# Performance work log

Measured on AMD Instinct MI355X. Metric: run time of the kernel, lower is better.

The kernel has to match this reference:

```python
import jax, jax.numpy as jnp
import numpy as np
import math

B, S, HID, H = 4, 2048, 1024, 16
D = HID // H


def setup_inputs() -> dict:
    key = jax.random.key(0)
    ks = jax.random.split(key, 13)
    xavier = lambda k: jax.random.normal(k, (HID, HID), jnp.float32) * math.sqrt(2.0 / (HID + HID))
    return {
        "q": jax.random.normal(ks[0], (B, S, HID), jnp.float32),
        "k": jax.random.normal(ks[1], (B, S, HID), jnp.float32),
        "v": jax.random.normal(ks[2], (B, S, HID), jnp.float32),
        "padding_mask": jax.random.randint(ks[3], (B, S), 0, 2, jnp.int32),
        "Wq": xavier(ks[4]), "bq": jnp.zeros((HID,), jnp.float32),
        "Wk": xavier(ks[5]), "bk": jnp.zeros((HID,), jnp.float32),
        "Wv": xavier(ks[6]), "bv": jnp.zeros((HID,), jnp.float32),
        "Wo": xavier(ks[7]), "bo": jnp.zeros((HID,), jnp.float32),
        "is_causal": 1,
    }


def reference(q, k, v, padding_mask, Wq, bq, Wk, bk, Wv, bv, Wo, bo, is_causal):
    b, s, _ = q.shape
    # torch Linear: y = x @ W.T + b; reshape to [B, H, S, D]
    proj = lambda x, W, bias: (x @ W.T + bias).reshape(b, s, H, D).transpose(0, 2, 1, 3)
    qh, kh, vh = proj(q, Wq, bq), proj(k, Wk, bk), proj(v, Wv, bv)
    corr = jnp.einsum("bhqd,bhkd->bhqk", qh, kh) / math.sqrt(D)  # [B,H,S,S]
    # padding_mask.view(B,1,S,1): masks QUERY rows where mask == 0 (faithful to source)
    corr = jnp.where(padding_mask[:, None, :, None] == 0, jnp.float32(-1e9), corr)
    if is_causal:
        # triu -inf above diagonal; where(...) equals corr + (-inf) at masked slots
        tri = jnp.triu(jnp.ones((s, s), bool), k=1)
        corr = jnp.where(tri[None, None], -jnp.inf, corr)
    prob = jax.nn.softmax(corr, axis=-1)  # dropout p=0 (eval)
    hidden = jnp.einsum("bhqk,bhkd->bhqd", prob, vh)  # [B,H,S,D]
    hidden = hidden.transpose(0, 2, 1, 3).reshape(b, s, H * D)
    return hidden @ Wo.T + bo
```

## Files before the change

### kernel.cpp

```cpp
#include <hip/hip_runtime.h>
#include <hip/hip_bf16.h>
#include <stdint.h>

typedef __attribute__((ext_vector_type(8))) short bf16x8;
typedef __attribute__((ext_vector_type(4))) float f32x4;
typedef __attribute__((ext_vector_type(16))) float f32x16;
typedef __attribute__((ext_vector_type(8))) unsigned short ushort8;
typedef __attribute__((ext_vector_type(4))) unsigned short ushort4v;
typedef __attribute__((ext_vector_type(4))) unsigned int u32x4;
typedef __attribute__((ext_vector_type(2))) unsigned int u32x2;

#define DEVINL __device__ __forceinline__

static constexpr int BB  = 4;
static constexpr int SS  = 2048;
static constexpr int HID = 1024;
static constexpr int NH  = 16;
static constexpr int DH  = 64;

DEVINL unsigned short f2bf(float f) {
  unsigned u = __builtin_bit_cast(unsigned, f);
  u += 0x7fffu + ((u >> 16) & 1u);
  return (unsigned short)(u >> 16);
}

DEVINL unsigned cvt_pk_bf16(float lo, float hi) {
  unsigned r;
  asm("v_cvt_pk_bf16_f32 %0, %1, %2" : "=v"(r) : "v"(lo), "v"(hi));
  return r;
}

DEVINL void gload_lds16(const void* g, void* lds) {
  __builtin_amdgcn_global_load_lds(
      (__attribute__((address_space(1))) unsigned int*)(g),
      (__attribute__((address_space(3))) unsigned int*)(lds), 16, 0, 0);
}

__global__ void cvt4_weights(const float* __restrict__ a,
                             const float* __restrict__ b,
                             const float* __restrict__ c,
                             const float* __restrict__ d,
                             unsigned short* __restrict__ dst) {
  int which = blockIdx.x >> 9;
  const float* src = which == 0 ? a : which == 1 ? b : which == 2 ? c : d;
  int i = ((blockIdx.x & 511) * 256 + threadIdx.x) * 8;
  float4 v0 = *(const float4*)(src + i);
  float4 v1 = *(const float4*)(src + i + 4);
  ushort8 h;
  h[0] = f2bf(v0.x); h[1] = f2bf(v0.y); h[2] = f2bf(v0.z); h[3] = f2bf(v0.w);
  h[4] = f2bf(v1.x); h[5] = f2bf(v1.y); h[6] = f2bf(v1.z); h[7] = f2bf(v1.w);
  *(ushort8*)(dst + which * 1048576 + i) = h;
}

__launch_bounds__(256)
__global__ void gemm_qkv(const float* __restrict__ qp,
                         const float* __restrict__ kp,
                         const float* __restrict__ vp,
                         const unsigned short* __restrict__ W,
                         const float* __restrict__ bq,
                         const float* __restrict__ bk,
                         const float* __restrict__ bv,
                         unsigned short* __restrict__ dstQK,
                         unsigned short* __restrict__ Vt, float sclq) {
  __shared__ __align__(16) unsigned char As[16384];
  __shared__ __align__(16) unsigned char Bs[2][16384];
  const int cpx = gridDim.x >> 3;
  const int bid = (blockIdx.x & 7) * cpx + (blockIdx.x >> 3);
  const int which = bid / 512;
  const int tile = bid - which * 512;
  const int bm = tile >> 3, bn = tile & 7;
  const int m0 = bm << 7, n0 = bn << 7;
  const int K = 1024, N = 1024;
  const float* Af = which == 0 ? qp : which == 1 ? kp : vp;
  const unsigned short* Bw = W + which * 1048576;
  const float* bias = which == 0 ? bq : which == 1 ? bk : bv;
  const float osc = which == 0 ? sclq : 1.0f;

  const int t = threadIdx.x, lane = t & 63, wv = t >> 6;
  const int wr = wv >> 1, wc = wv & 1;
  const int l15 = lane & 15, l4 = lane >> 4;

  f32x4 acc[4][4] = {};
  float4 ar[8];

  auto LOAD_A = [&](int k0) {
#pragma unroll
    for (int j = 0; j < 8; ++j) {
      int qid = t + j * 256;
      int row = qid >> 4;
      int q16 = qid & 15;
      ar[j] = *(const float4*)(Af + (size_t)(m0 + row) * K + k0 + q16 * 4);
    }
  };
  auto WRITE_A = [&]() {
#pragma unroll
    for (int j = 0; j < 8; ++j) {
      int qid = t + j * 256;
      int row = qid >> 4;
      int q16 = qid & 15;
      u32x2 w;
      w.x = cvt_pk_bf16(ar[j].x, ar[j].y);
      w.y = cvt_pk_bf16(ar[j].z, ar[j].w);
      int byte = (row * 128 + q16 * 8) ^ ((row & 7) << 4);
      *(u32x2*)(As + byte) = w;
    }
  };
  auto STAGE_B = [&](int k0, int s) {
#pragma unroll
    for (int j = 0; j < 4; ++j) {
      int p = (wv * 4 + j) * 1024 + lane * 16;
      int row = p >> 7;
      int cb = (p & 127) ^ ((row & 7) << 4);
      gload_lds16(Bw + (size_t)(n0 + row) * K + k0 + (cb >> 1),
                  Bs[s] + (wv * 4 + j) * 1024);
    }
  };

  LOAD_A(0);
  STAGE_B(0, 0);
  const int nk = K >> 6;
  for (int i = 0; i < nk; ++i) {
    const int s = i & 1;
    WRITE_A();
    if (i + 1 < nk) {
      LOAD_A((i + 1) << 6);
      STAGE_B((i + 1) << 6, s ^ 1);
      asm volatile("s_waitcnt vmcnt(12) lgkmcnt(0)" ::: "memory");
    } else {
      asm volatile("s_waitcnt vmcnt(0) lgkmcnt(0)" ::: "memory");
    }
    __builtin_amdgcn_s_barrier();

    bf16x8 af[2][4], bfr[2][4];
#pragma unroll
    for (int kh = 0; kh < 2; ++kh) {
#pragma unroll
      for (int m = 0; m < 4; ++m) {
        int r = wr * 64 + m * 16 + l15;
        int byte = (r * 128 + kh * 64 + l4 * 16) ^ ((r & 7) << 4);
        af[kh][m] = *(const bf16x8*)(As + byte);
      }
#pragma unroll
      for (int n = 0; n < 4; ++n) {
        int r = wc * 64 + n * 16 + l15;
        int byte = (r * 128 + kh * 64 + l4 * 16) ^ ((r & 7) << 4);
        bfr[kh][n] = *(const bf16x8*)(Bs[s] + byte);
      }
    }
#pragma unroll
    for (int kh = 0; kh < 2; ++kh)
#pragma unroll
      for (int m = 0; m < 4; ++m)
#pragma unroll
        for (int n = 0; n < 4; ++n)
          acc[m][n] = __builtin_amdgcn_mfma_f32_16x16x32_bf16(
              af[kh][m], bfr[kh][n], acc[m][n], 0, 0, 0);

    asm volatile("s_waitcnt lgkmcnt(0)" ::: "memory");
    __builtin_amdgcn_s_barrier();
  }

  if (which < 2) {
    unsigned short* Cp = dstQK + (size_t)which * 8388608;
#pragma unroll
    for (int n = 0; n < 4; ++n) {
      int col = n0 + wc * 64 + n * 16 + l15;
      float bc = bias[col];
#pragma unroll
      for (int m = 0; m < 4; ++m) {
        int rowb = m0 + wr * 64 + m * 16 + l4 * 4;
#pragma unroll
        for (int r = 0; r < 4; ++r) {
          float val = (acc[m][n][r] + bc) * osc;
          Cp[(size_t)(rowb + r) * N + col] = f2bf(val);
        }
      }
    }
  } else {
#pragma unroll
    for (int n = 0; n < 4; ++n) {
      int dcol = n0 + wc * 64 + n * 16 + l15;
      float bc = bias[dcol];
#pragma unroll
      for (int m = 0; m < 4; ++m) {
        int srow = m0 + wr * 64 + m * 16 + l4 * 4;
        int bb = srow >> 11, s = srow & 2047;
        ushort4v o;
#pragma unroll
        for (int r = 0; r < 4; ++r) o[r] = f2bf(acc[m][n][r] + bc);
        *(ushort4v*)(Vt + ((size_t)(bb * 1024 + dcol)) * 2048 + s) = o;
      }
    }
  }
}

__launch_bounds__(256)
__global__ void gemm_out(const unsigned short* __restrict__ Ab,
                         const unsigned short* __restrict__ Bw,
                         const float* __restrict__ bias,
                         float* __restrict__ Cp, int M, int N, int K) {
  __shared__ __align__(16) unsigned char As[2][16384];
  __shared__ __align__(16) unsigned char Bs[2][16384];
  const int cpx = gridDim.x >> 3;
  const int bid = (blockIdx.x & 7) * cpx + (blockIdx.x >> 3);
  const int nb = N >> 7;
  const int bm = bid / nb, bn = bid % nb;
  const int m0 = bm << 7, n0 = bn << 7;
  const int t = threadIdx.x, lane = t & 63, wv = t >> 6;
  const int wr = wv >> 1, wc = wv & 1;
  const int l15 = lane & 15, l4 = lane >> 4;

  f32x4 acc[4][4] = {};

  auto STAGE = [&](int k0, int s) {
#pragma unroll
    for (int j = 0; j < 4; ++j) {
      int p = (wv * 4 + j) * 1024 + lane * 16;
      int row = p >> 7;
      int cb = (p & 127) ^ ((row & 7) << 4);
      gload_lds16(Bw + (size_t)(n0 + row) * K + k0 + (cb >> 1),
                  Bs[s] + (wv * 4 + j) * 1024);
      gload_lds16(Ab + (size_t)(m0 + row) * K + k0 + (cb >> 1),
                  As[s] + (wv * 4 + j) * 1024);
    }
  };

  STAGE(0, 0);
  const int nk = K >> 6;
  for (int i = 0; i < nk; ++i) {
    const int s = i & 1;
    if (i + 1 < nk) {
      STAGE((i + 1) << 6, s ^ 1);
      asm volatile("s_waitcnt vmcnt(8)" ::: "memory");
    } else {
      asm volatile("s_waitcnt vmcnt(0)" ::: "memory");
    }
    __builtin_amdgcn_s_barrier();

    bf16x8 af[2][4], bfr[2][4];
#pragma unroll
    for (int kh = 0; kh < 2; ++kh) {
#pragma unroll
      for (int m = 0; m < 4; ++m) {
        int r = wr * 64 + m * 16 + l15;
        int byte = (r * 128 + kh * 64 + l4 * 16) ^ ((r & 7) << 4);
        af[kh][m] = *(const bf16x8*)(As[s] + byte);
      }
#pragma unroll
      for (int n = 0; n < 4; ++n) {
        int r = wc * 64 + n * 16 + l15;
        int byte = (r * 128 + kh * 64 + l4 * 16) ^ ((r & 7) << 4);
        bfr[kh][n] = *(const bf16x8*)(Bs[s] + byte);
      }
    }
#pragma unroll
    for (int kh = 0; kh < 2; ++kh)
#pragma unroll
      for (int m = 0; m < 4; ++m)
#pragma unroll
        for (int n = 0; n < 4; ++n)
          acc[m][n] = __builtin_amdgcn_mfma_f32_16x16x32_bf16(
              af[kh][m], bfr[kh][n], acc[m][n], 0, 0, 0);

    asm volatile("s_waitcnt lgkmcnt(0)" ::: "memory");
    __builtin_amdgcn_s_barrier();
  }

#pragma unroll
  for (int n = 0; n < 4; ++n) {
    int col = n0 + wc * 64 + n * 16 + l15;
    float bc = bias[col];
#pragma unroll
    for (int m = 0; m < 4; ++m) {
      int rowb = m0 + wr * 64 + m * 16 + l4 * 4;
#pragma unroll
      for (int r = 0; r < 4; ++r)
        Cp[(size_t)(rowb + r) * N + col] = acc[m][n][r] + bc;
    }
  }
}

__launch_bounds__(256)
__global__ void attn_kernel(const unsigned short* __restrict__ Qh,
                            const unsigned short* __restrict__ Kh,
                            const unsigned short* __restrict__ Vt,
                            const int* __restrict__ pad,
                            const int* __restrict__ pcausal,
                            unsigned short* __restrict__ Out) {
  __shared__ __align__(16) unsigned char Ks[2][16384];
  __shared__ __align__(16) unsigned char Vs[2][16384];
  const int bid = (blockIdx.x & 7) * 64 + (blockIdx.x >> 3);
  const int pr = bid & 7, h = (bid >> 3) & 15, b = bid >> 7;
  const int t = threadIdx.x, lane = t & 63, wv = t >> 6;
  const int l31 = lane & 31, hi = lane >> 5;
  const int causal = *pcausal;

  for (int half = 0; half < 2; ++half) {
    const int qt = half ? (15 - pr) : pr;
    const int q0 = qt << 7;
    const int qrow = q0 + wv * 32 + l31;
    const bool padded = (pad[b * SS + qrow] == 0);

    const unsigned short* Qb = Qh + ((size_t)(b * SS) + qrow) * HID + h * DH;
    bf16x8 qf[4];
#pragma unroll
    for (int dd = 0; dd < 4; ++dd) {
      qf[dd] = *(const bf16x8*)(Qb + dd * 16 + hi * 8);
      if (padded) qf[dd] = (bf16x8)0;
    }

    f32x16 oacc[2] = {};
    float m = -__builtin_inff(), l = 0.f;
    const int nkt = causal ? (qt + 1) : (SS >> 7);

    auto STAGE = [&](int kt, int s) {
#pragma unroll
      for (int j = 0; j < 4; ++j) {
        int p = (wv * 4 + j) * 1024 + lane * 16;
        int kr = p >> 7;
        int kcb = (p & 127) ^ ((kr & 7) << 4);
        gload_lds16(Kh + ((size_t)(b * SS) + (kt << 7) + kr) * HID + h * DH +
                        (kcb >> 1),
                    Ks[s] + (wv * 4 + j) * 1024);
        int vr = p >> 8;
        int vcb = (p & 255) ^ ((vr & 15) << 4);
        gload_lds16(Vt + ((size_t)((b * NH + h) * DH + vr)) * SS + (kt << 7) +
                        (vcb >> 1),
                    Vs[s] + (wv * 4 + j) * 1024);
      }
    };

    if (half) __syncthreads();
    STAGE(0, 0);
    for (int kt = 0; kt < nkt; ++kt) {
      asm volatile("s_waitcnt vmcnt(0)" ::: "memory");
      __syncthreads();
      if (kt + 1 < nkt) STAGE(kt + 1, (kt + 1) & 1);
      const unsigned char* Kb = Ks[kt & 1];
      const unsigned char* Vb = Vs[kt & 1];

#pragma unroll
      for (int sub = 0; sub < 2; ++sub) {
        const int k0 = (kt << 7) + (sub << 6);
        const bool active = (!causal) || (k0 <= q0 + wv * 32 + 31);
        if (!active) continue;
        f32x16 sacc[2] = {};
#pragma unroll
        for (int kb = 0; kb < 2; ++kb) {
#pragma unroll
          for (int dd = 0; dd < 4; ++dd) {
            int krow = sub * 64 + kb * 32 + l31;
            int byte = (krow * 128 + dd * 32 + hi * 16) ^ ((krow & 7) << 4);
            bf16x8 kf = *(const bf16x8*)(Kb + byte);
            sacc[kb] = __builtin_amdgcn_mfma_f32_32x32x16_bf16(kf, qf[dd],
                                                               sacc[kb], 0, 0, 0);
          }
        }
        if (causal && (k0 + 63 > q0 + wv * 32)) {
#pragma unroll
          for (int kb = 0; kb < 2; ++kb)
#pragma unroll
            for (int r = 0; r < 16; ++r) {
              int kidx = k0 + kb * 32 + (r & 3) + 8 * (r >> 2) + 4 * hi;
              if (kidx > qrow) sacc[kb][r] = -__builtin_inff();
            }
        }
        float ta = fmaxf(sacc[0][0], sacc[0][1]);
        float tb = fmaxf(sacc[0][2], sacc[0][3]);
#pragma unroll
        for (int r = 4; r < 16; r += 4) {
          ta = fmaxf(ta, fmaxf(sacc[0][r], sacc[0][r + 1]));
          tb = fmaxf(tb, fmaxf(sacc[0][r + 2], sacc[0][r + 3]));
        }
#pragma unroll
        for (int r = 0; r < 16; r += 4) {
          ta = fmaxf(ta, fmaxf(sacc[1][r], sacc[1][r + 1]));
          tb = fmaxf(tb, fmaxf(sacc[1][r + 2], sacc[1][r + 3]));
        }
        float tmax = fmaxf(ta, tb);
        tmax = fmaxf(tmax, __shfl_xor(tmax, 32));
        if (__any(tmax > m + 8.0f)) {
          float mnew = fmaxf(m, tmax);
          float corr = __builtin_amdgcn_exp2f(m - mnew);
          m = mnew;
          l *= corr;
#pragma unroll
          for (int db = 0; db < 2; ++db)
#pragma unroll
            for (int r = 0; r < 16; ++r) oacc[db][r] *= corr;
        }
        float ls = 0.f;
#pragma unroll
        for (int kb = 0; kb < 2; ++kb)
#pragma unroll
          for (int r = 0; r < 16; ++r) {
            float p = __builtin_amdgcn_exp2f(sacc[kb][r] - m);
            sacc[kb][r] = p;
            ls += p;
          }
        l += ls;

        bf16x8 pf[4];
#pragma unroll
        for (int kb = 0; kb < 2; ++kb) {
          unsigned w0 = cvt_pk_bf16(sacc[kb][0], sacc[kb][1]);
          unsigned w1 = cvt_pk_bf16(sacc[kb][2], sacc[kb][3]);
          unsigned w2 = cvt_pk_bf16(sacc[kb][4], sacc[kb][5]);
          unsigned w3 = cvt_pk_bf16(sacc[kb][6], sacc[kb][7]);
          unsigned w4 = cvt_pk_bf16(sacc[kb][8], sacc[kb][9]);
          unsigned w5 = cvt_pk_bf16(sacc[kb][10], sacc[kb][11]);
          unsigned w6 = cvt_pk_bf16(sacc[kb][12], sacc[kb][13]);
          unsigned w7 = cvt_pk_bf16(sacc[kb][14], sacc[kb][15]);
          unsigned t0 = __shfl_xor(hi ? w0 : w2, 32);
          unsigned t1 = __shfl_xor(hi ? w1 : w3, 32);
          unsigned t2 = __shfl_xor(hi ? w4 : w6, 32);
          unsigned t3 = __shfl_xor(hi ? w5 : w7, 32);
          u32x4 lo, hf;
          lo[0] = hi ? t0 : w0;
          lo[1] = hi ? t1 : w1;
          lo[2] = hi ? w2 : t0;
          lo[3] = hi ? w3 : t1;
          hf[0] = hi ? t2 : w4;
          hf[1] = hi ? t3 : w5;
          hf[2] = hi ? w6 : t2;
          hf[3] = hi ? w7 : t3;
          pf[2 * kb] = __builtin_bit_cast(bf16x8, lo);
          pf[2 * kb + 1] = __builtin_bit_cast(bf16x8, hf);
        }
#pragma unroll
        for (int db = 0; db < 2; ++db) {
#pragma unroll
          for (int kk = 0; kk < 4; ++kk) {
            int drow = db * 32 + l31;
            int byte = (drow * 256 + sub * 128 + kk * 32 + hi * 16) ^
                       ((drow & 15) << 4);
            bf16x8 vf = *(const bf16x8*)(Vb + byte);
            oacc[db] = __builtin_amdgcn_mfma_f32_32x32x16_bf16(vf, pf[kk],
                                                               oacc[db], 0, 0, 0);
          }
        }
      }
    }

    float ltot = l + __shfl_xor(l, 32);
    float inv = 1.0f / ltot;
    size_t rowoff = ((size_t)(b * SS) + qrow) * HID + h * DH;
#pragma unroll
    for (int db = 0; db < 2; ++db) {
#pragma unroll
      for (int g = 0; g < 4; ++g) {
        ushort4v o;
#pragma unroll
        for (int j = 0; j < 4; ++j) o[j] = f2bf(oacc[db][4 * g + j] * inv);
        *(ushort4v*)(Out + rowoff + db * 32 + 8 * g + 4 * hi) = o;
      }
    }
  }
}

extern "C" void kernel_launch(void* const* d_in, const int* in_sizes, int n_in,
                              void* d_out, int out_size, void* d_ws,
                              size_t ws_size, hipStream_t stream) {
  const float* q = (const float*)d_in[0];
  const float* k = (const float*)d_in[1];
  const float* v = (const float*)d_in[2];
  const int* pad = (const int*)d_in[3];
  const float* Wq = (const float*)d_in[4];
  const float* bq = (const float*)d_in[5];
  const float* Wk = (const float*)d_in[6];
  const float* bk = (const float*)d_in[7];
  const float* Wv = (const float*)d_in[8];
  const float* bv = (const float*)d_in[9];
  const float* Wo = (const float*)d_in[10];
  const float* bo = (const float*)d_in[11];
  const int* iscausal = (const int*)d_in[12];
  float* out = (float*)d_out;

  const float SCL = 0.18033688011112042f;
  const int NQKV = BB * SS * HID;

  unsigned short* Wcat = (unsigned short*)d_ws;
  unsigned short* Wob = Wcat + 3145728;
  unsigned short* Qh = Wob + 1048576;
  unsigned short* Kh = Qh + (size_t)NQKV;
  unsigned short* Vtp = Kh + (size_t)NQKV;
  unsigned short* Htmp = Vtp + (size_t)NQKV;

  cvt4_weights<<<2048, 256, 0, stream>>>(Wq, Wk, Wv, Wo, Wcat);

  gemm_qkv<<<1536, 256, 0, stream>>>(q, k, v, Wcat, bq, bk, bv, Qh, Vtp, SCL);

  attn_kernel<<<512, 256, 0, stream>>>(Qh, Kh, Vtp, pad, iscausal, Htmp);

  gemm_out<<<512, 256, 0, stream>>>(Htmp, Wob, bo, out, 8192, 1024, 1024);
}
```

Before: 179.0 us.

## Pre-convert QKV activations to bf16 and use double-buffered bf16 projection GEMMs

Adds a kernel that converts the fp32 q/k/v activations to bf16 up front, plus a new GEMM that streams both operands into double-buffered LDS with async global-to-LDS loads. It replaces the fused fp32-input QKV projection with three launches of that GEMM, one per projection, when the workspace is large enough. The aim is to halve the operand bytes the GEMM loads and to pipeline both operands, instead of converting fp32 A tiles inside the GEMM. The cost is an extra full read and write pass over the activations, more kernel launches and a larger workspace requirement. The old path is kept as a fallback.

After: 192.1 us. 1.07x slower.

```diff
diff --git a/kernel.cpp b/kernel.cpp
--- a/kernel.cpp
+++ b/kernel.cpp
@@ -50,6 +50,129 @@
   h[0] = f2bf(v0.x); h[1] = f2bf(v0.y); h[2] = f2bf(v0.z); h[3] = f2bf(v0.w);
   h[4] = f2bf(v1.x); h[5] = f2bf(v1.y); h[6] = f2bf(v1.z); h[7] = f2bf(v1.w);
   *(ushort8*)(dst + which * 1048576 + i) = h;
+}
+
+__global__ void cvt_qkv3(const float* __restrict__ q,
+                         const float* __restrict__ k,
+                         const float* __restrict__ v,
+                         unsigned short* __restrict__ dst) {
+  int which = blockIdx.x >> 12;
+  const float* src = which == 0 ? q : which == 1 ? k : v;
+  int i = ((blockIdx.x & 4095) * 256 + threadIdx.x) * 8;
+  float4 v0 = *(const float4*)(src + i);
+  float4 v1 = *(const float4*)(src + i + 4);
+  ushort8 h;
+  h[0] = f2bf(v0.x); h[1] = f2bf(v0.y); h[2] = f2bf(v0.z); h[3] = f2bf(v0.w);
+  h[4] = f2bf(v1.x); h[5] = f2bf(v1.y); h[6] = f2bf(v1.z); h[7] = f2bf(v1.w);
+  *(ushort8*)(dst + (size_t)which * 8388608 + i) = h;
+}
+
+__launch_bounds__(256)
+__global__ void gemm_b(const unsigned short* __restrict__ Ab,
+                       const unsigned short* __restrict__ Bw,
+                       const float* __restrict__ bias,
+                       unsigned short* __restrict__ dstN,
+                       unsigned short* __restrict__ dstT,
+                       int mode, float osc) {
+  __shared__ __align__(16) unsigned char As[2][16384];
+  __shared__ __align__(16) unsigned char Bs[2][16384];
+  const int K = 1024, N = 1024;
+  const int cpx = gridDim.x >> 3;
+  const int bid = (blockIdx.x & 7) * cpx + (blockIdx.x >> 3);
+  const int nb = N >> 7;
+  const int bm = bid / nb, bn = bid % nb;
+  const int m0 = bm << 7, n0 = bn << 7;
+  const int t = threadIdx.x, lane = t & 63, wv = t >> 6;
+  const int wr = wv >> 1, wc = wv & 1;
+  const int l15 = lane & 15, l4 = lane >> 4;
+
+  f32x4 acc[4][4] = {};
+
+  auto STAGE = [&](int k0, int s) {
+#pragma unroll
+    for (int j = 0; j < 4; ++j) {
+      int p = (wv * 4 + j) * 1024 + lane * 16;
+      int row = p >> 7;
+      int cb = (p & 127) ^ ((row & 7) << 4);
+      gload_lds16(Bw + (size_t)(n0 + row) * K + k0 + (cb >> 1),
+                  Bs[s] + (wv * 4 + j) * 1024);
+      gload_lds16(Ab + (size_t)(m0 + row) * K + k0 + (cb >> 1),
+                  As[s] + (wv * 4 + j) * 1024);
+    }
+  };
+
+  STAGE(0, 0);
+  const int nk = K >> 6;
+  for (int i = 0; i < nk; ++i) {
+    const int s = i & 1;
+    if (i + 1 < nk) {
+      STAGE((i + 1) << 6, s ^ 1);
+      asm volatile("s_waitcnt vmcnt(8)" ::: "memory");
+    } else {
+      asm volatile("s_waitcnt vmcnt(0)" ::: "memory");
+    }
+    __builtin_amdgcn_s_barrier();
+
+    bf16x8 af[2][4], bfr[2][4];
+#pragma unroll
+    for (int kh = 0; kh < 2; ++kh) {
+#pragma unroll
+      for (int m = 0; m < 4; ++m) {
+        int r = wr * 64 + m * 16 + l15;
+        int byte = (r * 128 + kh * 64 + l4 * 16) ^ ((r & 7) << 4);
+        af[kh][m] = *(const bf16x8*)(As[s] + byte);
+      }
+#pragma unroll
+      for (int n = 0; n < 4; ++n) {
+        int r = wc * 64 + n * 16 + l15;
+        int byte = (r * 128 + kh * 64 + l4 * 16) ^ ((r & 7) << 4);
+        bfr[kh][n] = *(const bf16x8*)(Bs[s] + byte);
+      }
+    }
+#pragma unroll
+    for (int kh = 0; kh < 2; ++kh)
+#pragma unroll
+      for (int m = 0; m < 4; ++m)
+#pragma unroll
+        for (int n = 0; n < 4; ++n)
+          acc[m][n] = __builtin_amdgcn_mfma_f32_16x16x32_bf16(
+              af[kh][m], bfr[kh][n], acc[m][n], 0, 0, 0);
+
+    asm volatile("s_waitcnt lgkmcnt(0)" ::: "memory");
+    __builtin_amdgcn_s_barrier();
+  }
+
+  if (mode == 0) {
+#pragma unroll
+    for (int n = 0; n < 4; ++n) {
+      int col = n0 + wc * 64 + n * 16 + l15;
+      float bc = bias[col];
+#pragma unroll
+      for (int m = 0; m < 4; ++m) {
+        int rowb = m0 + wr * 64 + m * 16 + l4 * 4;
+#pragma unroll
+        for (int r = 0; r < 4; ++r) {
+          float val = (acc[m][n][r] + bc) * osc;
+          dstN[(size_t)(rowb + r) * N + col] = f2bf(val);
+        }
+      }
+    }
+  } else {
+#pragma unroll
+    for (int n = 0; n < 4; ++n) {
+      int dcol = n0 + wc * 64 + n * 16 + l15;
+      float bc = bias[dcol];
+#pragma unroll
+      for (int m = 0; m < 4; ++m) {
+        int srow = m0 + wr * 64 + m * 16 + l4 * 4;
+        int bb = srow >> 11, s = srow & 2047;
+        ushort4v o;
+#pragma unroll
+        for (int r = 0; r < 4; ++r) o[r] = f2bf(acc[m][n][r] + bc);
+        *(ushort4v*)(dstT + ((size_t)(bb * 1024 + dcol)) * 2048 + s) = o;
+      }
+    }
+  }
 }
 
 __launch_bounds__(256)
@@ -477,20 +600,38 @@
   float* out = (float*)d_out;
 
   const float SCL = 0.18033688011112042f;
-  const int NQKV = BB * SS * HID;
-
-  unsigned short* Wcat = (unsigned short*)d_ws;
-  unsigned short* Wob = Wcat + 3145728;
-  unsigned short* Qh = Wob + 1048576;
-  unsigned short* Kh = Qh + (size_t)NQKV;
-  unsigned short* Vtp = Kh + (size_t)NQKV;
-  unsigned short* Htmp = Vtp + (size_t)NQKV;
-
-  cvt4_weights<<<2048, 256, 0, stream>>>(Wq, Wk, Wv, Wo, Wcat);
-
-  gemm_qkv<<<1536, 256, 0, stream>>>(q, k, v, Wcat, bq, bk, bv, Qh, Vtp, SCL);
-
-  attn_kernel<<<512, 256, 0, stream>>>(Qh, Kh, Vtp, pad, iscausal, Htmp);
-
-  gemm_out<<<512, 256, 0, stream>>>(Htmp, Wob, bo, out, 8192, 1024, 1024);
-}
+  const size_t NQ = 8388608;
+
+  if (ws_size >= 109051904ull) {
+    unsigned short* Wcat = (unsigned short*)d_ws;
+    unsigned short* Wob = Wcat + 3145728;
+    unsigned short* QKVb = Wob + 1048576;
+    unsigned short* Qh = QKVb + 3 * NQ;
+    unsigned short* Kh = Qh + NQ;
+    unsigned short* Vtp = Kh + NQ;
+    unsigned short* Htmp = QKVb;
+
+    cvt4_weights<<<2048, 256, 0, stream>>>(Wq, Wk, Wv, Wo, Wcat);
+    cvt_qkv3<<<12288, 256, 0, stream>>>(q, k, v, QKVb);
+    gemm_b<<<512, 256, 0, stream>>>(QKVb, Wcat, bq, Qh, nullptr, 0, SCL);
+    gemm_b<<<512, 256, 0, stream>>>(QKVb + NQ, Wcat + 1048576, bk, Kh, nullptr,
+                                    0, 1.0f);
+    gemm_b<<<512, 256, 0, stream>>>(QKVb + 2 * NQ, Wcat + 2097152, bv, nullptr,
+                                    Vtp, 1, 1.0f);
+    attn_kernel<<<512, 256, 0, stream>>>(Qh, Kh, Vtp, pad, iscausal, Htmp);
+    gemm_out<<<512, 256, 0, stream>>>(Htmp, Wob, bo, out, 8192, 1024, 1024);
+  } else {
+    unsigned short* Wcat = (unsigned short*)d_ws;
+    unsigned short* Wob = Wcat + 3145728;
+    unsigned short* Qh = Wob + 1048576;
+    unsigned short* Kh = Qh + NQ;
+    unsigned short* Vtp = Kh + NQ;
+    unsigned short* Htmp = Vtp + NQ;
+
+    cvt4_weights<<<2048, 256, 0, stream>>>(Wq, Wk, Wv, Wo, Wcat);
+    gemm_qkv<<<1536, 256, 0, stream>>>(q, k, v, Wcat, bq, bk, bv, Qh, Vtp,
+                                       SCL);
+    attn_kernel<<<512, 256, 0, stream>>>(Qh, Kh, Vtp, pad, iscausal, Htmp);
+    gemm_out<<<512, 256, 0, stream>>>(Htmp, Wob, bo, out, 8192, 1024, 1024);
+  }
+}
```
